# Optimization experiments

Measured on AMD Instinct MI355X. Metric: run time of the kernel, lower is better.

The kernel has to match this reference:

```python
import jax, jax.numpy as jnp
import numpy as np

N_NODES = 50000
N_EDGES = 600000
DIM_H = 128
LN_EPS = 1e-5


def setup_inputs() -> dict:
    key = jax.random.key(0)
    ks = jax.random.split(key, 8)
    s = 1.0 / np.sqrt(DIM_H)
    return {
        "nodes": jax.random.normal(ks[0], (N_NODES, DIM_H), jnp.float32),
        "W_msg": jax.random.normal(ks[1], (DIM_H, DIM_H), jnp.float32) * s,
        "b_msg": jnp.zeros((DIM_H,), jnp.float32),
        "w_ih": jax.random.normal(ks[2], (3 * DIM_H, DIM_H), jnp.float32) * s,
        "w_hh": jax.random.normal(ks[3], (3 * DIM_H, DIM_H), jnp.float32) * s,
        "b_ih": jnp.zeros((3 * DIM_H,), jnp.float32),
        "b_hh": jnp.zeros((3 * DIM_H,), jnp.float32),
        "ln_gamma": jnp.ones((DIM_H,), jnp.float32),
        "ln_beta": jnp.zeros((DIM_H,), jnp.float32),
        "edge_src": jax.random.randint(ks[4], (N_EDGES,), 0, N_NODES, jnp.int32),
        "edge_dst": jax.random.randint(ks[5], (N_EDGES,), 0, N_NODES, jnp.int32),
    }


def _layer_norm(x, gamma, beta):
    mu = jnp.mean(x, axis=-1, keepdims=True)
    var = jnp.mean(jnp.square(x - mu), axis=-1, keepdims=True)
    return gamma * (x - mu) * jax.lax.rsqrt(var + LN_EPS) + beta


def reference(nodes, W_msg, b_msg, w_ih, w_hh, b_ih, b_hh, ln_gamma, ln_beta,
              edge_src, edge_dst):
    n_nodes = nodes.shape[0]
    # send_and_recv: per-edge message from source node, sum-reduce at dest
    msg_e = nodes[edge_src] @ W_msg.T + b_msg            # [E, H] (irregular gather)
    messages = jax.ops.segment_sum(msg_e, edge_dst, num_segments=n_nodes)  # [N, H]
    # global connection: add mean node feature
    msg = messages + jnp.mean(nodes, axis=0)
    # single-step GRU (torch gate layout: r, z, n)
    gi = msg @ w_ih.T + b_ih                             # [N, 3H]
    gh = nodes @ w_hh.T + b_hh                           # [N, 3H]
    i_r, i_z, i_n = jnp.split(gi, 3, axis=-1)
    h_r, h_z, h_n = jnp.split(gh, 3, axis=-1)
    r = jax.nn.sigmoid(i_r + h_r)
    z = jax.nn.sigmoid(i_z + h_z)
    n = jnp.tanh(i_n + r * h_n)
    h_next = (1.0 - z) * n + z * nodes
    # LayerNorm then post-GRU spatial residual with messages
    out = _layer_norm(h_next, ln_gamma, ln_beta)
    out = out + messages
    return out
```

## Files before the change

### kernel.cpp

```cpp
#include <hip/hip_runtime.h>
#include <hip/hip_bf16.h>

#define N_NODES 50000
#define N_EDGES 600000
#define DIM_H   128
#define NPAD    50048
#define NB_SCAN 196

typedef __attribute__((ext_vector_type(8))) short bf16x8;
typedef __attribute__((ext_vector_type(4))) float f32x4;
typedef __attribute__((ext_vector_type(4))) short short4v;

__device__ __forceinline__ float b2f(__hip_bfloat16 x) { return __bfloat162float(x); }
__device__ __forceinline__ short f2bs(float f) {
    __hip_bfloat16 h = __float2bfloat16(f);
    return *reinterpret_cast<short*>(&h);
}
__device__ __forceinline__ float bs2f(short s) {
    unsigned u = ((unsigned)(unsigned short)s) << 16;
    return __builtin_bit_cast(float, u);
}

__device__ __forceinline__ void dma16(const void* g, const void* lds_uniform) {
    __builtin_amdgcn_global_load_lds(
        (const __attribute__((address_space(1))) void*)g,
        (__attribute__((address_space(3))) void*)(unsigned)(unsigned long long)lds_uniform,
        16, 0, 0);
}

__global__ __launch_bounds__(256) void colsum_k(const float* __restrict__ nodes,
                                                float* __restrict__ colsum,
                                                short* __restrict__ nodesB) {
    __shared__ float red[8][128];
    const int tid = threadIdx.x;
    const int cg = tid & 31;
    const int rl = tid >> 5;
    float4 acc = {0.f, 0.f, 0.f, 0.f};
    for (int r = blockIdx.x * 8 + rl; r < N_NODES; r += gridDim.x * 8) {
        float4 v = *(const float4*)(nodes + (size_t)r * DIM_H + cg * 4);
        acc.x += v.x; acc.y += v.y; acc.z += v.z; acc.w += v.w;
        *(short4v*)(nodesB + (size_t)r * DIM_H + cg * 4) =
            (short4v){f2bs(v.x), f2bs(v.y), f2bs(v.z), f2bs(v.w)};
    }
    *(float4*)&red[rl][cg * 4] = acc;
    __syncthreads();
    if (tid < 128) {
        float s = 0.f;
#pragma unroll
        for (int i = 0; i < 8; ++i) s += red[i][tid];
        unsafeAtomicAdd(&colsum[tid], s);
    }
}

__global__ __launch_bounds__(256) void wcvt_k(const float* __restrict__ wmsg,
                                              const float* __restrict__ wih,
                                              const float* __restrict__ whh,
                                              short* __restrict__ wmsgB,
                                              short* __restrict__ wihB,
                                              short* __restrict__ whhB) {
    int i = blockIdx.x * 256 + threadIdx.x;
    if (i < 16384) wmsgB[i] = f2bs(wmsg[i]);
    if (i < 49152) { wihB[i] = f2bs(wih[i]); whhB[i] = f2bs(whh[i]); }
}

__global__ __launch_bounds__(256) void hist_k(const int* __restrict__ edst,
                                              int* __restrict__ cnt) {
    int e = blockIdx.x * 256 + threadIdx.x;
    if (e < N_EDGES) atomicAdd(&cnt[edst[e]], 1);
}

__global__ __launch_bounds__(256) void bsum_k(const int* __restrict__ cnt,
                                              int* __restrict__ bsum) {
    const int t = threadIdx.x;
    int i = blockIdx.x * 256 + t;
    int v = (i < N_NODES) ? cnt[i] : 0;
#pragma unroll
    for (int o = 32; o; o >>= 1) v += __shfl_xor(v, o, 64);
    __shared__ int w4[4];
    if ((t & 63) == 0) w4[t >> 6] = v;
    __syncthreads();
    if (t == 0) bsum[blockIdx.x] = w4[0] + w4[1] + w4[2] + w4[3];
}

__global__ __launch_bounds__(256) void scan2_k(const int* __restrict__ cnt,
                                               const int* __restrict__ bsum,
                                               int* __restrict__ rowptr,
                                               int* __restrict__ pos) {
    const int b = blockIdx.x, t = threadIdx.x;
    const int lane = t & 63, w = t >> 6;
    __shared__ int red[4];
    __shared__ int wsum[4];

    int ov = (t < b) ? bsum[t] : 0;
#pragma unroll
    for (int o = 32; o; o >>= 1) ov += __shfl_xor(ov, o, 64);
    if (lane == 0) red[w] = ov;
    __syncthreads();
    const int offset = red[0] + red[1] + red[2] + red[3];

    int i = b * 256 + t;
    int v = (i < N_NODES) ? cnt[i] : 0;
    int x = v;
#pragma unroll
    for (int o = 1; o < 64; o <<= 1) {
        int y = __shfl_up(x, o, 64);
        if (lane >= o) x += y;
    }
    if (lane == 63) wsum[w] = x;
    __syncthreads();
    int woff = 0;
#pragma unroll
    for (int j = 0; j < 4; ++j)
        if (j < w) woff += wsum[j];
    int excl = offset + woff + (x - v);
    if (i < N_NODES) { rowptr[i] = excl; pos[i] = excl; }
    if (i == N_NODES - 1) rowptr[N_NODES] = excl + v;
}

__global__ __launch_bounds__(256) void reorder_k(const int* __restrict__ esrc,
                                                 const int* __restrict__ edst,
                                                 int* __restrict__ pos,
                                                 int* __restrict__ ssrc) {
    int e = blockIdx.x * 256 + threadIdx.x;
    if (e < N_EDGES) {
        int p = atomicAdd(&pos[edst[e]], 1);
        ssrc[p] = esrc[e];
    }
}

__global__ __launch_bounds__(256) void aggregate_k(const short* __restrict__ nodesB,
                                                   const int* __restrict__ rowptr,
                                                   const int* __restrict__ ssrc,
                                                   short* __restrict__ aggB) {
    const int wid = threadIdx.x >> 6;
    const int lane = threadIdx.x & 63;
    const int n = blockIdx.x * 4 + wid;
    if (n >= N_NODES) return;
    const int s0 = rowptr[n], s1 = rowptr[n + 1];
    float2 acc = {0.f, 0.f};
    int e = s0;
    for (; e + 3 < s1; e += 4) {
        int sa = ssrc[e], sb = ssrc[e + 1], sc = ssrc[e + 2], sd = ssrc[e + 3];
        short2 va = ((const short2*)(nodesB + (size_t)sa * DIM_H))[lane];
        short2 vb = ((const short2*)(nodesB + (size_t)sb * DIM_H))[lane];
        short2 vc = ((const short2*)(nodesB + (size_t)sc * DIM_H))[lane];
        short2 vd = ((const short2*)(nodesB + (size_t)sd * DIM_H))[lane];
        acc.x += (bs2f(va.x) + bs2f(vb.x)) + (bs2f(vc.x) + bs2f(vd.x));
        acc.y += (bs2f(va.y) + bs2f(vb.y)) + (bs2f(vc.y) + bs2f(vd.y));
    }
    for (; e < s1; ++e) {
        int sa = ssrc[e];
        short2 va = ((const short2*)(nodesB + (size_t)sa * DIM_H))[lane];
        acc.x += bs2f(va.x);
        acc.y += bs2f(va.y);
    }
    short2 o; o.x = f2bs(acc.x); o.y = f2bs(acc.y);
    ((short2*)(aggB + (size_t)n * DIM_H))[lane] = o;
}

__device__ __forceinline__ void stage_tile(const short* __restrict__ src, int row0,
                                           short* lds, int w, int lane) {
#pragma unroll
    for (int it = 0; it < 8; ++it) {
        int c = w * 8 + it;
        int s = c * 64 + lane;
        int r = s >> 4, q = s & 15;
        int g = q ^ (r & 15);
        dma16(src + (((size_t)(row0 + r)) << 7) + (g << 3), lds + (size_t)c * 512);
    }
}

__global__ __launch_bounds__(256) void mgemm0_k(const short* __restrict__ aggB,
                                                const short* __restrict__ wmsgB,
                                                const float* __restrict__ bmsg,
                                                const int* __restrict__ degi,
                                                const float* __restrict__ colsum,
                                                short* __restrict__ msginB) {
    __shared__ short As[128 * 128];
    __shared__ short Ws[128 * 128];
    const int tid = threadIdx.x;
    const int lane = tid & 63, w = tid >> 6;
    const int m0 = blockIdx.x * 128;

    stage_tile(aggB, m0, As, w, lane);
    stage_tile(wmsgB, 0, Ws, w, lane);
    __syncthreads();

    const int r16 = lane & 15, half = lane >> 4;
    const int wm = (w >> 1) * 64, wn = (w & 1) * 64;
    f32x4 acc[4][4] = {};
#pragma unroll
    for (int kt = 0; kt < 4; ++kt) {
        const int sq = ((kt * 4 + half) ^ r16) << 3;
        bf16x8 af[4], bfr[4];
#pragma unroll
        for (int t = 0; t < 4; ++t) {
            af[t]  = *(const bf16x8*)&As[(wm + t * 16 + r16) * 128 + sq];
            bfr[t] = *(const bf16x8*)&Ws[(wn + t * 16 + r16) * 128 + sq];
        }
#pragma unroll
        for (int i = 0; i < 4; ++i)
#pragma unroll
            for (int j = 0; j < 4; ++j)
                acc[i][j] = __builtin_amdgcn_mfma_f32_16x16x32_bf16(
                    af[i], bfr[j], acc[i][j], 0, 0, 0);
    }

#pragma unroll
    for (int i = 0; i < 4; ++i)
#pragma unroll
        for (int r = 0; r < 4; ++r) {
            int m = m0 + wm + i * 16 + half * 4 + r;
            if (m < N_NODES) {
#pragma unroll
                for (int j = 0; j < 4; ++j) {
                    int n = wn + j * 16 + r16;
                    float c = acc[i][j][r] + (float)degi[m] * bmsg[n]
                            + colsum[n] * (1.0f / N_NODES);
                    msginB[(size_t)m * 128 + n] = f2bs(c);
                }
            }
        }
}

__global__ __launch_bounds__(256) void gigh_k(const short* __restrict__ msginB,
                                              const short* __restrict__ nodesB,
                                              const short* __restrict__ wihB,
                                              const short* __restrict__ whhB,
                                              const float* __restrict__ bih,
                                              const float* __restrict__ bhh,
                                              short* __restrict__ gi,
                                              short* __restrict__ gh) {
    __shared__ short As[128 * 128];
    __shared__ short Ws[128 * 128];
    const int tid = threadIdx.x;
    const int lane = tid & 63, w = tid >> 6;
    const int m0 = blockIdx.x * 128;
    const int y = blockIdx.y;
    const short* A; const short* W; const float* bias; short* out; int n0;
    if (y < 3) { A = msginB; W = wihB; bias = bih; out = gi; n0 = y * 128; }
    else       { A = nodesB; W = whhB; bias = bhh; out = gh; n0 = (y - 3) * 128; }

    stage_tile(A, m0, As, w, lane);
    stage_tile(W, n0, Ws, w, lane);
    __syncthreads();

    const int r16 = lane & 15, half = lane >> 4;
    const int wm = (w >> 1) * 64, wn = (w & 1) * 64;
    f32x4 acc[4][4] = {};
#pragma unroll
    for (int kt = 0; kt < 4; ++kt) {
        const int sq = ((kt * 4 + half) ^ r16) << 3;
        bf16x8 af[4], bfr[4];
#pragma unroll
        for (int t = 0; t < 4; ++t) {
            af[t]  = *(const bf16x8*)&As[(wm + t * 16 + r16) * 128 + sq];
            bfr[t] = *(const bf16x8*)&Ws[(wn + t * 16 + r16) * 128 + sq];
        }
#pragma unroll
        for (int i = 0; i < 4; ++i)
#pragma unroll
            for (int j = 0; j < 4; ++j)
                acc[i][j] = __builtin_amdgcn_mfma_f32_16x16x32_bf16(
                    af[i], bfr[j], acc[i][j], 0, 0, 0);
    }

#pragma unroll
    for (int i = 0; i < 4; ++i)
#pragma unroll
        for (int r = 0; r < 4; ++r) {
            int m = m0 + wm + i * 16 + half * 4 + r;
            if (m < N_NODES) {
#pragma unroll
                for (int j = 0; j < 4; ++j) {
                    int n = n0 + wn + j * 16 + r16;
                    out[(size_t)m * 384 + n] = f2bs(acc[i][j][r] + bias[n]);
                }
            }
        }
}

__global__ __launch_bounds__(256) void fuse_k(const float* __restrict__ nodes,
                                              const __hip_bfloat16* __restrict__ gi,
                                              const __hip_bfloat16* __restrict__ gh,
                                              const __hip_bfloat16* __restrict__ msginB,
                                              const float* __restrict__ colsum,
                                              const float* __restrict__ gamma,
                                              const float* __restrict__ beta,
                                              float* __restrict__ out) {
    const int wid = threadIdx.x >> 6;
    const int lane = threadIdx.x & 63;
    const int n = blockIdx.x * 4 + wid;
    if (n >= N_NODES) return;

    const __hip_bfloat16* gir = gi + (size_t)n * 384;
    const __hip_bfloat16* ghr = gh + (size_t)n * 384;

    float hn[2], resid[2];
    float s = 0.f;
#pragma unroll
    for (int t = 0; t < 2; ++t) {
        int c = lane + t * 64;
        float ir = b2f(gir[c]), iz = b2f(gir[128 + c]), inn = b2f(gir[256 + c]);
        float hr = b2f(ghr[c]), hz = b2f(ghr[128 + c]), hhn = b2f(ghr[256 + c]);
        float r = 1.f / (1.f + expf(-(ir + hr)));
        float z = 1.f / (1.f + expf(-(iz + hz)));
        float ng = tanhf(inn + r * hhn);
        float h = nodes[(size_t)n * DIM_H + c];
        hn[t] = (1.f - z) * ng + z * h;
        float mi = b2f(msginB[(size_t)n * DIM_H + c]);
        resid[t] = mi - colsum[c] * (1.0f / N_NODES);
        s += hn[t];
    }
#pragma unroll
    for (int o = 32; o; o >>= 1) s += __shfl_xor(s, o, 64);
    float mu = s * (1.0f / DIM_H);
    float v = 0.f;
#pragma unroll
    for (int t = 0; t < 2; ++t) {
        float d = hn[t] - mu;
        v += d * d;
    }
#pragma unroll
    for (int o = 32; o; o >>= 1) v += __shfl_xor(v, o, 64);
    float rstd = rsqrtf(v * (1.0f / DIM_H) + 1e-5f);
#pragma unroll
    for (int t = 0; t < 2; ++t) {
        int c = lane + t * 64;
        float y = gamma[c] * (hn[t] - mu) * rstd + beta[c];
        out[(size_t)n * DIM_H + c] = y + resid[t];
    }
}

extern "C" void kernel_launch(void* const* d_in, const int* in_sizes, int n_in,
                              void* d_out, int out_size, void* d_ws, size_t ws_size,
                              hipStream_t stream) {
    const float* nodes = (const float*)d_in[0];
    const float* Wmsg  = (const float*)d_in[1];
    const float* bmsg  = (const float*)d_in[2];
    const float* wih   = (const float*)d_in[3];
    const float* whh   = (const float*)d_in[4];
    const float* bih   = (const float*)d_in[5];
    const float* bhh   = (const float*)d_in[6];
    const float* gamma = (const float*)d_in[7];
    const float* beta  = (const float*)d_in[8];
    const int* esrc = (const int*)d_in[9];
    const int* edst = (const int*)d_in[10];
    float* out = (float*)d_out;

    char* ws = (char*)d_ws;
    short* gi_s   = (short*)ws;
    short* aggB   = (short*)ws;
    short* gh_s   = (short*)(ws + 38400000);
    int*   bsum   = (int*)(ws + 38400000);
    short* nodesB = (short*)(ws + 76800000);
    short* msginB = (short*)(ws + 89612288);
    short* wmsgB  = (short*)(ws + 102424576);
    short* wihB   = (short*)(ws + 102457344);
    short* whhB   = (short*)(ws + 102555648);
    float* colsum = (float*)(ws + 102653952);
    int*   cnt    = (int*)(ws + 102654464);
    int*   rowptr = (int*)(ws + 102854464);
    int*   pos    = (int*)(ws + 103054472);
    int*   ssrc   = (int*)(ws + 103254472);

    hipMemsetAsync(cnt, 0, N_NODES * sizeof(int), stream);
    hipMemsetAsync(colsum, 0, DIM_H * sizeof(float), stream);
    hipMemsetAsync(ws + (size_t)N_NODES * 256, 0, (NPAD - N_NODES) * 256, stream);
    hipMemsetAsync(ws + 76800000 + (size_t)N_NODES * 256, 0, (NPAD - N_NODES) * 256, stream);
    hipMemsetAsync(ws + 89612288 + (size_t)N_NODES * 256, 0, (NPAD - N_NODES) * 256, stream);

    colsum_k<<<512, 256, 0, stream>>>(nodes, colsum, nodesB);
    wcvt_k<<<192, 256, 0, stream>>>(Wmsg, wih, whh, wmsgB, wihB, whhB);

    const int EB = (N_EDGES + 255) / 256;
    hist_k<<<EB, 256, 0, stream>>>(edst, cnt);
    bsum_k<<<NB_SCAN, 256, 0, stream>>>(cnt, bsum);
    scan2_k<<<NB_SCAN, 256, 0, stream>>>(cnt, bsum, rowptr, pos);
    reorder_k<<<EB, 256, 0, stream>>>(esrc, edst, pos, ssrc);
    aggregate_k<<<(N_NODES + 3) / 4, 256, 0, stream>>>(nodesB, rowptr, ssrc, aggB);

    const int MB2 = (N_NODES + 127) / 128;
    mgemm0_k<<<dim3(MB2, 1), 256, 0, stream>>>(aggB, wmsgB, bmsg, cnt, colsum, msginB);
    gigh_k<<<dim3(MB2, 6), 256, 0, stream>>>(msginB, nodesB, wihB, whhB, bih, bhh,
                                             gi_s, gh_s);

    fuse_k<<<(N_NODES + 3) / 4, 256, 0, stream>>>(nodes,
                                                  (const __hip_bfloat16*)gi_s,
                                                  (const __hip_bfloat16*)gh_s,
                                                  (const __hip_bfloat16*)msginB,
                                                  colsum, gamma, beta, out);
}
```

Before: 281.1 us.

## Fold memsets into prep kernel and vectorize GRU/LayerNorm epilogue

Replaces five hipMemsetAsync calls and the weight-conversion kernel with one prep kernel that zeroes counters, colsum and pad tails, cutting launch overhead. The fuse kernel now loads packed short2/float2 values, reads bf16 nodes instead of fp32, and computes LayerNorm variance in one pass as E[x^2]-mu^2. The workspace layout is rearranged so buffers no longer alias. The trade-off is slightly lower precision from bf16 hidden state and the one-pass variance.

After: 271.1 us. 3.6% less time.

```diff
diff --git a/kernel.cpp b/kernel.cpp
--- a/kernel.cpp
+++ b/kernel.cpp
@@ -11,7 +11,6 @@
 typedef __attribute__((ext_vector_type(4))) float f32x4;
 typedef __attribute__((ext_vector_type(4))) short short4v;
 
-__device__ __forceinline__ float b2f(__hip_bfloat16 x) { return __bfloat162float(x); }
 __device__ __forceinline__ short f2bs(float f) {
     __hip_bfloat16 h = __float2bfloat16(f);
     return *reinterpret_cast<short*>(&h);
@@ -20,12 +19,37 @@
     unsigned u = ((unsigned)(unsigned short)s) << 16;
     return __builtin_bit_cast(float, u);
 }
+__device__ __forceinline__ float sigm(float x) { return 1.f / (1.f + expf(-x)); }
 
 __device__ __forceinline__ void dma16(const void* g, const void* lds_uniform) {
     __builtin_amdgcn_global_load_lds(
         (const __attribute__((address_space(1))) void*)g,
         (__attribute__((address_space(3))) void*)(unsigned)(unsigned long long)lds_uniform,
         16, 0, 0);
+}
+
+__global__ __launch_bounds__(256) void prep_k(const float* __restrict__ wmsg,
+                                              const float* __restrict__ wih,
+                                              const float* __restrict__ whh,
+                                              short* __restrict__ wmsgB,
+                                              short* __restrict__ wihB,
+                                              short* __restrict__ whhB,
+                                              int* __restrict__ cnt,
+                                              float* __restrict__ colsum,
+                                              short* __restrict__ aggTail,
+                                              short* __restrict__ nodesTail,
+                                              short* __restrict__ msginTail) {
+    int i = blockIdx.x * 256 + threadIdx.x;
+    if (i < 16384) wmsgB[i] = f2bs(wmsg[i]);
+    if (i < 49152) { wihB[i] = f2bs(wih[i]); whhB[i] = f2bs(whh[i]); }
+    if (i < N_NODES) cnt[i] = 0;
+    if (i < 128) colsum[i] = 0.f;
+    if (i < 1536) {
+        short4v z = {0, 0, 0, 0};
+        *(short4v*)(aggTail   + i * 4) = z;
+        *(short4v*)(nodesTail + i * 4) = z;
+        *(short4v*)(msginTail + i * 4) = z;
+    }
 }
 
 __global__ __launch_bounds__(256) void colsum_k(const float* __restrict__ nodes,
@@ -50,17 +74,6 @@
         for (int i = 0; i < 8; ++i) s += red[i][tid];
         unsafeAtomicAdd(&colsum[tid], s);
     }
-}
-
-__global__ __launch_bounds__(256) void wcvt_k(const float* __restrict__ wmsg,
-                                              const float* __restrict__ wih,
-                                              const float* __restrict__ whh,
-                                              short* __restrict__ wmsgB,
-                                              short* __restrict__ wihB,
-                                              short* __restrict__ whhB) {
-    int i = blockIdx.x * 256 + threadIdx.x;
-    if (i < 16384) wmsgB[i] = f2bs(wmsg[i]);
-    if (i < 49152) { wihB[i] = f2bs(wih[i]); whhB[i] = f2bs(whh[i]); }
 }
 
 __global__ __launch_bounds__(256) void hist_k(const int* __restrict__ edst,
@@ -170,6 +183,28 @@
     }
 }
 
+__device__ __forceinline__ void wave_mm(const short* __restrict__ A,
+                                        const short* __restrict__ W,
+                                        f32x4 (&acc)[4][4],
+                                        int wm, int wn, int r16, int half) {
+#pragma unroll
+    for (int kt = 0; kt < 4; ++kt) {
+        const int sq = ((kt * 4 + half) ^ r16) << 3;
+        bf16x8 af[4], bfr[4];
+#pragma unroll
+        for (int t = 0; t < 4; ++t) {
+            af[t]  = *(const bf16x8*)&A[(wm + t * 16 + r16) * 128 + sq];
+            bfr[t] = *(const bf16x8*)&W[(wn + t * 16 + r16) * 128 + sq];
+        }
+#pragma unroll
+        for (int i = 0; i < 4; ++i)
+#pragma unroll
+            for (int j = 0; j < 4; ++j)
+                acc[i][j] = __builtin_amdgcn_mfma_f32_16x16x32_bf16(
+                    af[i], bfr[j], acc[i][j], 0, 0, 0);
+    }
+}
+
 __global__ __launch_bounds__(256) void mgemm0_k(const short* __restrict__ aggB,
                                                 const short* __restrict__ wmsgB,
                                                 const float* __restrict__ bmsg,
@@ -189,22 +224,7 @@
     const int r16 = lane & 15, half = lane >> 4;
     const int wm = (w >> 1) * 64, wn = (w & 1) * 64;
     f32x4 acc[4][4] = {};
-#pragma unroll
-    for (int kt = 0; kt < 4; ++kt) {
-        const int sq = ((kt * 4 + half) ^ r16) << 3;
-        bf16x8 af[4], bfr[4];
-#pragma unroll
-        for (int t = 0; t < 4; ++t) {
-            af[t]  = *(const bf16x8*)&As[(wm + t * 16 + r16) * 128 + sq];
-            bfr[t] = *(const bf16x8*)&Ws[(wn + t * 16 + r16) * 128 + sq];
-        }
-#pragma unroll
-        for (int i = 0; i < 4; ++i)
-#pragma unroll
-            for (int j = 0; j < 4; ++j)
-                acc[i][j] = __builtin_amdgcn_mfma_f32_16x16x32_bf16(
-                    af[i], bfr[j], acc[i][j], 0, 0, 0);
-    }
+    wave_mm(As, Ws, acc, wm, wn, r16, half);
 
 #pragma unroll
     for (int i = 0; i < 4; ++i)
@@ -248,22 +268,7 @@
     const int r16 = lane & 15, half = lane >> 4;
     const int wm = (w >> 1) * 64, wn = (w & 1) * 64;
     f32x4 acc[4][4] = {};
-#pragma unroll
-    for (int kt = 0; kt < 4; ++kt) {
-        const int sq = ((kt * 4 + half) ^ r16) << 3;
-        bf16x8 af[4], bfr[4];
-#pragma unroll
-        for (int t = 0; t < 4; ++t) {
-            af[t]  = *(const bf16x8*)&As[(wm + t * 16 + r16) * 128 + sq];
-            bfr[t] = *(const bf16x8*)&Ws[(wn + t * 16 + r16) * 128 + sq];
-        }
-#pragma unroll
-        for (int i = 0; i < 4; ++i)
-#pragma unroll
-            for (int j = 0; j < 4; ++j)
-                acc[i][j] = __builtin_amdgcn_mfma_f32_16x16x32_bf16(
-                    af[i], bfr[j], acc[i][j], 0, 0, 0);
-    }
+    wave_mm(As, Ws, acc, wm, wn, r16, half);
 
 #pragma unroll
     for (int i = 0; i < 4; ++i)
@@ -280,10 +285,10 @@
         }
 }
 
-__global__ __launch_bounds__(256) void fuse_k(const float* __restrict__ nodes,
-                                              const __hip_bfloat16* __restrict__ gi,
-                                              const __hip_bfloat16* __restrict__ gh,
-                                              const __hip_bfloat16* __restrict__ msginB,
+__global__ __launch_bounds__(256) void fuse_k(const short* __restrict__ nodesB,
+                                              const short* __restrict__ gi,
+                                              const short* __restrict__ gh,
+                                              const short* __restrict__ msginB,
                                               const float* __restrict__ colsum,
                                               const float* __restrict__ gamma,
                                               const float* __restrict__ beta,
@@ -293,43 +298,50 @@
     const int n = blockIdx.x * 4 + wid;
     if (n >= N_NODES) return;
 
-    const __hip_bfloat16* gir = gi + (size_t)n * 384;
-    const __hip_bfloat16* ghr = gh + (size_t)n * 384;
+    const short* gir = gi + (size_t)n * 384;
+    const short* ghr = gh + (size_t)n * 384;
+
+    short2 ir2 = ((const short2*)gir)[lane];
+    short2 iz2 = ((const short2*)(gir + 128))[lane];
+    short2 in2 = ((const short2*)(gir + 256))[lane];
+    short2 hr2 = ((const short2*)ghr)[lane];
+    short2 hz2 = ((const short2*)(ghr + 128))[lane];
+    short2 hn2 = ((const short2*)(ghr + 256))[lane];
+    short2 h2  = ((const short2*)(nodesB + (size_t)n * DIM_H))[lane];
+    short2 mi2 = ((const short2*)(msginB + (size_t)n * DIM_H))[lane];
+    float2 cs2 = ((const float2*)colsum)[lane];
+    float2 ga2 = ((const float2*)gamma)[lane];
+    float2 be2 = ((const float2*)beta)[lane];
 
     float hn[2], resid[2];
-    float s = 0.f;
-#pragma unroll
-    for (int t = 0; t < 2; ++t) {
-        int c = lane + t * 64;
-        float ir = b2f(gir[c]), iz = b2f(gir[128 + c]), inn = b2f(gir[256 + c]);
-        float hr = b2f(ghr[c]), hz = b2f(ghr[128 + c]), hhn = b2f(ghr[256 + c]);
-        float r = 1.f / (1.f + expf(-(ir + hr)));
-        float z = 1.f / (1.f + expf(-(iz + hz)));
-        float ng = tanhf(inn + r * hhn);
-        float h = nodes[(size_t)n * DIM_H + c];
-        hn[t] = (1.f - z) * ng + z * h;
-        float mi = b2f(msginB[(size_t)n * DIM_H + c]);
-        resid[t] = mi - colsum[c] * (1.0f / N_NODES);
-        s += hn[t];
-    }
-#pragma unroll
-    for (int o = 32; o; o >>= 1) s += __shfl_xor(s, o, 64);
+    {
+        float r = sigm(bs2f(ir2.x) + bs2f(hr2.x));
+        float z = sigm(bs2f(iz2.x) + bs2f(hz2.x));
+        float ng = tanhf(bs2f(in2.x) + r * bs2f(hn2.x));
+        hn[0] = (1.f - z) * ng + z * bs2f(h2.x);
+        resid[0] = bs2f(mi2.x) - cs2.x * (1.0f / N_NODES);
+    }
+    {
+        float r = sigm(bs2f(ir2.y) + bs2f(hr2.y));
+        float z = sigm(bs2f(iz2.y) + bs2f(hz2.y));
+        float ng = tanhf(bs2f(in2.y) + r * bs2f(hn2.y));
+        hn[1] = (1.f - z) * ng + z * bs2f(h2.y);
+        resid[1] = bs2f(mi2.y) - cs2.y * (1.0f / N_NODES);
+    }
+    float s = hn[0] + hn[1];
+    float q = hn[0] * hn[0] + hn[1] * hn[1];
+#pragma unroll
+    for (int o = 32; o; o >>= 1) {
+        s += __shfl_xor(s, o, 64);
+        q += __shfl_xor(q, o, 64);
+    }
     float mu = s * (1.0f / DIM_H);
-    float v = 0.f;
-#pragma unroll
-    for (int t = 0; t < 2; ++t) {
-        float d = hn[t] - mu;
-        v += d * d;
-    }
-#pragma unroll
-    for (int o = 32; o; o >>= 1) v += __shfl_xor(v, o, 64);
-    float rstd = rsqrtf(v * (1.0f / DIM_H) + 1e-5f);
-#pragma unroll
-    for (int t = 0; t < 2; ++t) {
-        int c = lane + t * 64;
-        float y = gamma[c] * (hn[t] - mu) * rstd + beta[c];
-        out[(size_t)n * DIM_H + c] = y + resid[t];
-    }
+    float var = q * (1.0f / DIM_H) - mu * mu;
+    float rstd = rsqrtf(var + 1e-5f);
+    float2 o2;
+    o2.x = ga2.x * (hn[0] - mu) * rstd + be2.x + resid[0];
+    o2.y = ga2.y * (hn[1] - mu) * rstd + be2.y + resid[1];
+    ((float2*)(out + (size_t)n * DIM_H))[lane] = o2;
 }
 
 extern "C" void kernel_launch(void* const* d_in, const int* in_sizes, int n_in,
@@ -350,28 +362,27 @@
 
     char* ws = (char*)d_ws;
     short* gi_s   = (short*)ws;
-    short* aggB   = (short*)ws;
     short* gh_s   = (short*)(ws + 38400000);
-    int*   bsum   = (int*)(ws + 38400000);
-    short* nodesB = (short*)(ws + 76800000);
-    short* msginB = (short*)(ws + 89612288);
-    short* wmsgB  = (short*)(ws + 102424576);
-    short* wihB   = (short*)(ws + 102457344);
-    short* whhB   = (short*)(ws + 102555648);
-    float* colsum = (float*)(ws + 102653952);
-    int*   cnt    = (int*)(ws + 102654464);
-    int*   rowptr = (int*)(ws + 102854464);
-    int*   pos    = (int*)(ws + 103054472);
-    int*   ssrc   = (int*)(ws + 103254472);
-
-    hipMemsetAsync(cnt, 0, N_NODES * sizeof(int), stream);
-    hipMemsetAsync(colsum, 0, DIM_H * sizeof(float), stream);
-    hipMemsetAsync(ws + (size_t)N_NODES * 256, 0, (NPAD - N_NODES) * 256, stream);
-    hipMemsetAsync(ws + 76800000 + (size_t)N_NODES * 256, 0, (NPAD - N_NODES) * 256, stream);
-    hipMemsetAsync(ws + 89612288 + (size_t)N_NODES * 256, 0, (NPAD - N_NODES) * 256, stream);
-
+    short* aggB   = (short*)(ws + 76800000);
+    short* nodesB = (short*)(ws + 89612288);
+    short* msginB = (short*)(ws + 102424576);
+    short* wmsgB  = (short*)(ws + 115236864);
+    short* wihB   = (short*)(ws + 115269632);
+    short* whhB   = (short*)(ws + 115367936);
+    float* colsum = (float*)(ws + 115466240);
+    int*   cnt    = (int*)(ws + 115466752);
+    int*   rowptr = (int*)(ws + 115666752);
+    int*   pos    = (int*)(ws + 115866760);
+    int*   ssrc   = (int*)(ws + 116066760);
+    int*   bsum   = (int*)(ws + 118466760);
+
+    short* aggTail   = aggB   + (size_t)N_NODES * DIM_H;
+    short* nodesTail = nodesB + (size_t)N_NODES * DIM_H;
+    short* msginTail = msginB + (size_t)N_NODES * DIM_H;
+
+    prep_k<<<NB_SCAN, 256, 0, stream>>>(Wmsg, wih, whh, wmsgB, wihB, whhB,
+                                        cnt, colsum, aggTail, nodesTail, msginTail);
     colsum_k<<<512, 256, 0, stream>>>(nodes, colsum, nodesB);
-    wcvt_k<<<192, 256, 0, stream>>>(Wmsg, wih, whh, wmsgB, wihB, whhB);
 
     const int EB = (N_EDGES + 255) / 256;
     hist_k<<<EB, 256, 0, stream>>>(edst, cnt);
@@ -385,9 +396,6 @@
     gigh_k<<<dim3(MB2, 6), 256, 0, stream>>>(msginB, nodesB, wihB, whhB, bih, bhh,
                                              gi_s, gh_s);
 
-    fuse_k<<<(N_NODES + 3) / 4, 256, 0, stream>>>(nodes,
-                                                  (const __hip_bfloat16*)gi_s,
-                                                  (const __hip_bfloat16*)gh_s,
-                                                  (const __hip_bfloat16*)msginB,
+    fuse_k<<<(N_NODES + 3) / 4, 256, 0, stream>>>(nodesB, gi_s, gh_s, msginB,
                                                   colsum, gamma, beta, out);
 }
```
